# Optimization experiments

Measured on AMD Instinct MI355X. Metric: run time of the kernel, lower is better.

## Reference

```python
import jax, jax.numpy as jnp
import numpy as np


def _diag_perm(h, w):
    # Matches torch loop: offsets -(h-1)..w-1, within offset ordered by row i.
    ii, jj = np.meshgrid(np.arange(h), np.arange(w), indexing='ij')
    idx = np.lexsort((ii.ravel(), (jj - ii).ravel())).astype(np.int32)
    inv = np.argsort(idx).astype(np.int32)
    return jnp.asarray(idx), jnp.asarray(inv)


def _mamba(tok, ln_g, ln_b, Win, conv_w, conv_b, Wx, Wdt, bdt, A_log, Dp, Wout):
    # tok: (B, L, C). MambaLayer = LayerNorm + standard Mamba block.
    di, dc = conv_w.shape
    ds = A_log.shape[-1]
    dtr = Wdt.shape[-1]
    mu = tok.mean(-1, keepdims=True)
    var = ((tok - mu) ** 2).mean(-1, keepdims=True)
    t = (tok - mu) * jax.lax.rsqrt(var + 1e-5) * ln_g + ln_b
    xz = jnp.einsum('blc,ec->ble', t, Win)          # (B,L,2*di)
    xh, z = jnp.split(xz, 2, axis=-1)
    # causal depthwise conv over sequence
    xc = jnp.transpose(xh, (0, 2, 1))               # (B,di,L)
    xc = jax.lax.conv_general_dilated(
        xc, conv_w[:, None, :], (1,), [(dc - 1, 0)],
        dimension_numbers=('NCH', 'OIH', 'NCH'), feature_group_count=di)
    u = jax.nn.silu(jnp.transpose(xc, (0, 2, 1)) + conv_b)  # (B,L,di)
    proj = jnp.einsum('bld,ed->ble', u, Wx)
    dt_r, Bm, Cm = jnp.split(proj, [dtr, dtr + ds], axis=-1)
    dt = jax.nn.softplus(jnp.einsum('blr,dr->bld', dt_r, Wdt) + bdt)  # (B,L,di)
    A = -jnp.exp(A_log)                              # (di,ds)

    def step(h, inp):
        dt_t, B_t, C_t, u_t = inp                    # (B,di) (B,ds) (B,ds) (B,di)
        dA = jnp.exp(dt_t[..., None] * A)            # (B,di,ds)
        h = dA * h + dt_t[..., None] * B_t[:, None, :] * u_t[..., None]
        y = jnp.einsum('bds,bs->bd', h, C_t)
        return h, y

    h0 = jnp.zeros((u.shape[0], di, ds), u.dtype)
    _, ys = jax.lax.scan(step, h0, (jnp.moveaxis(dt, 1, 0), jnp.moveaxis(Bm, 1, 0),
                                    jnp.moveaxis(Cm, 1, 0), jnp.moveaxis(u, 1, 0)))
    y = jnp.moveaxis(ys, 0, 1) + u * Dp              # (B,L,di)
    y = y * jax.nn.silu(z)
    return jnp.einsum('bld,cd->blc', y, Wout)


def _forward(x, ln_g, ln_b, Win, conv_w, conv_b, Wx, Wdt, bdt, A_log, Dp, Wout):
    b, c, h, w = x.shape
    idx, inv = _diag_perm(h, w)

    def mam(d, tok):
        return _mamba(tok, ln_g[d], ln_b[d], Win[d], conv_w[d], conv_b[d],
                      Wx[d], Wdt[d], bdt[d], A_log[d], Dp[d], Wout[d])

    row_tok = x.reshape(b, c, h * w).transpose(0, 2, 1)
    row_feat = mam(0, row_tok).transpose(0, 2, 1).reshape(b, c, h, w)
    col_tok = x.transpose(0, 1, 3, 2).reshape(b, c, w * h).transpose(0, 2, 1)
    col_feat = mam(1, col_tok).transpose(0, 2, 1).reshape(b, c, w, h).transpose(0, 1, 3, 2)
    diag_feat = mam(2, row_tok[:, idx, :])[:, inv, :].transpose(0, 2, 1).reshape(b, c, h, w)
    xf = x[:, :, :, ::-1]
    anti_tok = xf.reshape(b, c, h * w).transpose(0, 2, 1)[:, idx, :]
    anti_feat = mam(3, anti_tok)[:, inv, :].transpose(0, 2, 1).reshape(b, c, h, w)[:, :, :, ::-1]
    gate = jax.nn.sigmoid((row_feat + col_feat + diag_feat + anti_feat) / 4.0)
    return x * gate


def setup_inputs() -> dict:
    key = jax.random.key(0)
    ks = jax.random.split(key, 8)
    B, C, H, W = 4, 96, 48, 48
    DI, DS, DC, DTR = 192, 16, 4, 6
    s = 0.05
    return {
        'x': jax.random.normal(ks[0], (B, C, H, W), jnp.float32),
        'ln_g': jnp.ones((4, C), jnp.float32),
        'ln_b': jnp.zeros((4, C), jnp.float32),
        'Win': jax.random.normal(ks[1], (4, 2 * DI, C), jnp.float32) * s,
        'conv_w': jax.random.normal(ks[2], (4, DI, DC), jnp.float32) * s,
        'conv_b': jnp.zeros((4, DI), jnp.float32),
        'Wx': jax.random.normal(ks[3], (4, DTR + 2 * DS, DI), jnp.float32) * s,
        'Wdt': jax.random.normal(ks[4], (4, DI, DTR), jnp.float32) * s,
        'bdt': jax.random.normal(ks[5], (4, DI), jnp.float32) * s,
        'A_log': jnp.log(jnp.broadcast_to(jnp.arange(1, DS + 1, dtype=jnp.float32), (4, DI, DS))),
        'Dp': jnp.ones((4, DI), jnp.float32),
        'Wout': jax.random.normal(ks[6], (4, C, DI), jnp.float32) * s,
    }


def reference(x, ln_g, ln_b, Win, conv_w, conv_b, Wx, Wdt, bdt, A_log, Dp, Wout):
    return _forward(x, ln_g, ln_b, Win, conv_w, conv_b, Wx, Wdt, bdt, A_log, Dp, Wout)
```

## Files before the change

### kernel.cpp

```cpp
#include <hip/hip_runtime.h>
#include <math.h>

#define LSEQ 2304
#define LC 32
#define NCH 72

typedef unsigned short u16;
typedef unsigned int u32;
typedef __attribute__((ext_vector_type(8))) short bf16x8;
typedef __attribute__((ext_vector_type(4))) float f32x4;

__device__ __forceinline__ float sigmoidf_(float v){ return 1.f/(1.f+__expf(-v)); }
__device__ __forceinline__ u16 f2b(float f){
  union{float f; u32 u;} v; v.f = f;
  u32 r = v.u + 0x7fffu + ((v.u >> 16) & 1u);
  return (u16)(r >> 16);
}
__device__ __forceinline__ float b2f(u16 h){
  union{u32 u; float f;} v; v.u = ((u32)h) << 16; return v.f;
}
__device__ __forceinline__ u16 f2h(float f){
  _Float16 h = (_Float16)f;
  union{_Float16 h; u16 u;} v; v.h = h; return v.u;
}
__device__ __forceinline__ float h2f(u16 u){
  union{u16 u; _Float16 h;} v; v.u = u; return (float)v.h;
}
__device__ __forceinline__ uint2 pack4(float a, float b, float c, float d){
  uint2 o;
  o.x = (u32)f2b(a) | ((u32)f2b(b) << 16);
  o.y = (u32)f2b(c) | ((u32)f2b(d) << 16);
  return o;
}
__device__ __forceinline__ float softplus_(float v){
  return fmaxf(v, 0.f) + __logf(1.f + __expf(-fabsf(v)));
}

__global__ void prep_fold(const float* __restrict__ Win, const float* __restrict__ ln_g,
                          const float* __restrict__ ln_b, const float* __restrict__ A_log,
                          const float* __restrict__ Wout, const float* __restrict__ Wx,
                          const float* __restrict__ Wdt, const float* __restrict__ bdt,
                          u16* __restrict__ WinMF, float* __restrict__ b2,
                          float* __restrict__ Aneg2, u16* __restrict__ WoutMF,
                          u16* __restrict__ Wcomb, float* __restrict__ bcomb,
                          int* __restrict__ g, int* __restrict__ invg, int* __restrict__ flag){
  int i = blockIdx.x * 256 + threadIdx.x;
  if (i < LSEQ){
    int l = i;
    g[l] = l;
    g[LSEQ + l] = (l % 48) * 48 + l / 48;
    invg[l] = l;
    invg[LSEQ + l] = (l % 48) * 48 + l / 48;
    int p = i;
    int ii = p / 48, jj = p % 48, dd = jj - ii;
    int off = (dd <= 0) ? (47 + dd) * (48 + dd) / 2
                        : 1176 + 48 * (dd - 1) - dd * (dd - 1) / 2;
    int l2 = off + min(ii, jj);
    g[2 * LSEQ + l2] = p;
    g[3 * LSEQ + l2] = ii * 48 + 47 - jj;
    invg[2 * LSEQ + p] = l2;
    invg[3 * LSEQ + ii * 48 + 47 - jj] = l2;
  }
  if (i < 4*192*16){
    float a = -expf(A_log[i]);
    Aneg2[i] = a * 1.44269504f;
    int s = i & 15;
    float a0 = -expf(A_log[i - s]);
    if (fabsf(a - (float)(s + 1) * a0) > 1e-5f * fabsf(a) + 1e-30f)
      atomicOr(flag, 1);
  }
  if (i < 4*384*96){
    int d = i / 36864, r = i % 36864, c = r % 96;
    WinMF[i] = f2b(Win[i] * ln_g[d*96 + c]);
  }
  if (i < 4*96*192) WoutMF[i] = f2b(Wout[i]);
  if (i < 4*224*192){
    int d = i / 43008, r = i % 43008, e = r / 192, c = r % 192;
    float w;
    if (e < 192){
      const float* wdt = &Wdt[(size_t)(d*192 + e) * 6];
      w = 0.f;
      #pragma unroll
      for (int r6 = 0; r6 < 6; ++r6) w += wdt[r6] * Wx[(size_t)(d*38 + r6) * 192 + c];
    } else if (e < 208){
      w = Wx[(size_t)(d*38 + 6 + (e - 192)) * 192 + c];
    } else {
      w = Wx[(size_t)(d*38 + 22 + (e - 208)) * 192 + c];
    }
    Wcomb[i] = f2b(w);
  }
  if (i < 4*224){
    int d = i / 224, e = i % 224;
    bcomb[i] = (e < 192) ? bdt[d*192 + e] : 0.f;
  }
  if (i < 4*384){
    int d = i / 384;
    const float* wr = &Win[(size_t)i * 96];
    const float* lb = &ln_b[d * 96];
    float s = 0.f;
    for (int c = 0; c < 96; ++c) s += wr[c] * lb[c];
    b2[i] = s;
  }
}

__global__ __launch_bounds__(256) void ln_kernel(const float* __restrict__ x, u16* __restrict__ n){
  __shared__ float red[512];
  int tid = threadIdx.x;
  int s = tid & 63, q = tid >> 6;
  int T = blockIdx.x * 64 + s;
  int b = T / 2304, p = T % 2304;
  const float* xp = x + (size_t)b * 96 * 2304 + p;
  float vals[24];
  float sum = 0.f, ss = 0.f;
  #pragma unroll
  for (int k = 0; k < 24; ++k){
    float v = xp[(size_t)(q*24 + k) * 2304];
    vals[k] = v; sum += v; ss += v*v;
  }
  red[q*64 + s] = sum;
  red[256 + q*64 + s] = ss;
  __syncthreads();
  float S = red[s] + red[64+s] + red[128+s] + red[192+s];
  float Q = red[256+s] + red[320+s] + red[384+s] + red[448+s];
  float mu = S * (1.f/96.f);
  float var = Q * (1.f/96.f) - mu*mu;
  float rs = rsqrtf(var + 1e-5f);
  u32 w[12];
  #pragma unroll
  for (int k = 0; k < 12; ++k){
    float v0 = (vals[2*k]   - mu) * rs;
    float v1 = (vals[2*k+1] - mu) * rs;
    w[k] = (u32)f2b(v0) | ((u32)f2b(v1) << 16);
  }
  uint4* np_ = (uint4*)(n + (size_t)T * 96 + q*24);
  np_[0] = make_uint4(w[0], w[1], w[2],  w[3]);
  np_[1] = make_uint4(w[4], w[5], w[6],  w[7]);
  np_[2] = make_uint4(w[8], w[9], w[10], w[11]);
}

__global__ __launch_bounds__(256) void kproj(const u16* __restrict__ nbf,
    const u16* __restrict__ WinMF, const float* __restrict__ b2,
    const int* __restrict__ invg, u16* __restrict__ xz, u16* __restrict__ sz){
  int d = blockIdx.y;
  int wv = threadIdx.x >> 6, lane = threadIdx.x & 63;
  int lr = lane & 15, lg = lane >> 4;
  int r0 = blockIdx.x * 64 + wv * 16;
  int row = r0 + lr;
  int b = row / 2304, p = row % 2304;
  const u16* Ap = nbf + (size_t)row * 96 + lg * 8;
  bf16x8 tk0 = *(const bf16x8*)(Ap);
  bf16x8 tk1 = *(const bf16x8*)(Ap + 32);
  bf16x8 tk2 = *(const bf16x8*)(Ap + 64);
  const u16* Wb = WinMF + (size_t)d * 36864 + (size_t)lr * 96 + lg * 8;
  const float* b2d = b2 + d * 384;
  u16* outx = xz + ((size_t)d * 9216 + row) * 192;
  int lseq = invg[d * LSEQ + p];
  u16* outz = sz + ((size_t)(d*4 + b) * LSEQ + lseq) * 192;
  for (int grp = 0; grp < 3; ++grp){
    f32x4 acc[8];
    #pragma unroll
    for (int t = 0; t < 8; ++t)
      acc[t] = *(const f32x4*)&b2d[(grp*8 + t)*16 + lg*4];
    #pragma unroll
    for (int t = 0; t < 8; ++t){
      const u16* wp = Wb + (size_t)(grp*8 + t) * 1536;
      acc[t] = __builtin_amdgcn_mfma_f32_16x16x32_bf16(*(const bf16x8*)(wp     ), tk0, acc[t], 0, 0, 0);
      acc[t] = __builtin_amdgcn_mfma_f32_16x16x32_bf16(*(const bf16x8*)(wp + 32), tk1, acc[t], 0, 0, 0);
      acc[t] = __builtin_amdgcn_mfma_f32_16x16x32_bf16(*(const bf16x8*)(wp + 64), tk2, acc[t], 0, 0, 0);
    }
    #pragma unroll
    for (int t = 0; t < 8; ++t){
      int te = grp*8 + t;
      if (te < 12){
        uint2 o = pack4(acc[t][0], acc[t][1], acc[t][2], acc[t][3]);
        *(uint2*)&outx[te*16 + lg*4] = o;
      } else {
        float z0 = acc[t][0], z1 = acc[t][1], z2 = acc[t][2], z3 = acc[t][3];
        z0 *= sigmoidf_(z0); z1 *= sigmoidf_(z1); z2 *= sigmoidf_(z2); z3 *= sigmoidf_(z3);
        *(uint2*)&outz[(te-12)*16 + lg*4] = pack4(z0, z1, z2, z3);
      }
    }
  }
}

__global__ __launch_bounds__(256) void kconv(const u16* __restrict__ xz, const int* __restrict__ g,
    const float* __restrict__ conv_w, const float* __restrict__ conv_b,
    u16* __restrict__ u){
  __shared__ u16 xh[67][200];
  int d = blockIdx.z, b = blockIdx.y, l0 = blockIdx.x * 64;
  int tid = threadIdx.x;
  const int* gd = g + d * LSEQ;
  const u16* xzd = xz + (size_t)d * 9216 * 192 + (size_t)b * LSEQ * 192;
  for (int i = tid; i < 67*24; i += 256){
    int lt = i / 24, j = i % 24;
    int gl = l0 - 3 + lt;
    uint4 v = make_uint4(0u, 0u, 0u, 0u);
    if (gl >= 0){
      int p = gd[gl];
      v = *(const uint4*)(xzd + (size_t)p * 192 + j * 8);
    }
    *(uint4*)&xh[lt][j*8] = v;
  }
  __syncthreads();
  size_t obase = ((size_t)(d*4 + b) * LSEQ + l0) * 192;
  for (int i = tid; i < 64*48; i += 256){
    int lt = i / 48, j = (i % 48) * 4;
    float a0 = conv_b[d*192 + j + 0];
    float a1 = conv_b[d*192 + j + 1];
    float a2 = conv_b[d*192 + j + 2];
    float a3 = conv_b[d*192 + j + 3];
    const float4 w0 = *(const float4*)&conv_w[(size_t)(d*192 + j + 0) * 4];
    const float4 w1 = *(const float4*)&conv_w[(size_t)(d*192 + j + 1) * 4];
    const float4 w2 = *(const float4*)&conv_w[(size_t)(d*192 + j + 2) * 4];
    const float4 w3 = *(const float4*)&conv_w[(size_t)(d*192 + j + 3) * 4];
    const float* w0p = (const float*)&w0;
    const float* w1p = (const float*)&w1;
    const float* w2p = (const float*)&w2;
    const float* w3p = (const float*)&w3;
    #pragma unroll
    for (int kk = 0; kk < 4; ++kk){
      uint2 xv = *(const uint2*)&xh[lt + kk][j];
      a0 += w0p[kk] * b2f((u16)(xv.x & 0xffff));
      a1 += w1p[kk] * b2f((u16)(xv.x >> 16));
      a2 += w2p[kk] * b2f((u16)(xv.y & 0xffff));
      a3 += w3p[kk] * b2f((u16)(xv.y >> 16));
    }
    a0 *= sigmoidf_(a0); a1 *= sigmoidf_(a1); a2 *= sigmoidf_(a2); a3 *= sigmoidf_(a3);
    *(uint2*)(u + obase + (size_t)lt * 192 + j) = pack4(a0, a1, a2, a3);
  }
}

__global__ __launch_bounds__(256) void kernBM(const u16* __restrict__ u,
    const u16* __restrict__ Wcomb, const float* __restrict__ bcomb,
    u16* __restrict__ dtb, float* __restrict__ Bm, float* __restrict__ Cm){
  __shared__ u16 ush[64 * 200];
  int d = blockIdx.y;
  int tid = threadIdx.x;
  int tile0 = blockIdx.x * 64;
  const u16* ub = u + ((size_t)d * 4 * LSEQ + tile0) * 192;
  for (int i = tid; i < 64*24; i += 256){
    int row = i / 24, c8 = i % 24;
    *(uint4*)&ush[row*200 + c8*8] = *(const uint4*)&ub[(size_t)row*192 + c8*8];
  }
  __syncthreads();
  int wv = tid >> 6, lane = tid & 63;
  int lr = lane & 15, lg = lane >> 4;
  const u16* urow = &ush[(wv*16 + lr)*200 + lg*8];
  bf16x8 tk[6];
  #pragma unroll
  for (int kc = 0; kc < 6; ++kc) tk[kc] = *(const bf16x8*)(urow + kc*32);
  const u16* Wb = Wcomb + (size_t)d * 224 * 192 + (size_t)lr * 192 + lg * 8;
  bf16x8 bw[2][6];
  #pragma unroll
  for (int kc = 0; kc < 6; ++kc) bw[0][kc] = *(const bf16x8*)(Wb + kc*32);
  size_t tokrow = (size_t)d * 4 * LSEQ + tile0 + wv*16 + lr;
  for (int t = 0; t < 14; ++t){
    int cur = t & 1;
    if (t < 13){
      const u16* wp = Wb + (size_t)(t + 1) * 3072;
      #pragma unroll
      for (int kc = 0; kc < 6; ++kc) bw[cur^1][kc] = *(const bf16x8*)(wp + kc*32);
    }
    f32x4 a = (f32x4){0.f, 0.f, 0.f, 0.f};
    #pragma unroll
    for (int kc = 0; kc < 6; ++kc)
      a = __builtin_amdgcn_mfma_f32_16x16x32_bf16(bw[cur][kc], tk[kc], a, 0, 0, 0);
    if (t < 12){
      f32x4 bb = *(const f32x4*)&bcomb[d*224 + t*16 + lg*4];
      float s0 = softplus_(a[0] + bb[0]);
      float s1 = softplus_(a[1] + bb[1]);
      float s2 = softplus_(a[2] + bb[2]);
      float s3 = softplus_(a[3] + bb[3]);
      uint2 o;
      o.x = (u32)f2h(s0) | ((u32)f2h(s1) << 16);
      o.y = (u32)f2h(s2) | ((u32)f2h(s3) << 16);
      *(uint2*)&dtb[tokrow * 192 + t*16 + lg*4] = o;
    } else if (t == 12){
      *(float4*)&Bm[tokrow * 16 + lg*4] = make_float4(a[0], a[1], a[2], a[3]);
    } else {
      *(float4*)&Cm[tokrow * 16 + lg*4] = make_float4(a[0], a[1], a[2], a[3]);
    }
  }
}

__global__ __launch_bounds__(192) void kernC1(const u16* __restrict__ dtb, const u16* __restrict__ u,
    const float* __restrict__ Bm, const float* __restrict__ Cm,
    const float* __restrict__ Aneg2, const int* __restrict__ flag,
    u16* __restrict__ hfin, float* __restrict__ Send, u32* __restrict__ yS){
  __shared__ float Bsh[LC*16];
  __shared__ float Csh[LC*16];
  __shared__ u16 dtsh[LC*192];
  __shared__ u16 ush2[LC*192];
  int ch = blockIdx.x, b = blockIdx.y, d = blockIdx.z;
  int seq = d*4 + b;
  int di = threadIdx.x;
  size_t tb = (size_t)seq * LSEQ + ch * LC;
  const float* bp = Bm + tb * 16;
  const float* cp = Cm + tb * 16;
  for (int i = di; i < LC*16; i += 192){ Bsh[i] = bp[i]; Csh[i] = cp[i]; }
  {
    const uint4* dt4 = (const uint4*)(dtb + tb * 192);
    const uint4* u4  = (const uint4*)(u   + tb * 192);
    #pragma unroll
    for (int i = di; i < LC*24; i += 192){
      *(uint4*)&dtsh[i*8] = dt4[i];
      *(uint4*)&ush2[i*8] = u4[i];
    }
  }
  u32* ySp = yS + tb * 192;
  float h[16];
  #pragma unroll
  for (int s = 0; s < 16; ++s) h[s] = 0.f;
  float Sacc = 0.f;
  __syncthreads();
  if (*flag == 0){
    float A2_0 = Aneg2[(d*192 + di) * 16];
    for (int j = 0; j < LC; ++j){
      float dtv = h2f(dtsh[j*192 + di]);
      float uv  = b2f(ush2[j*192 + di]);
      float Bs[16], Cs[16];
      {
        const float4* b4 = (const float4*)&Bsh[j * 16];
        const float4* c4 = (const float4*)&Csh[j * 16];
        #pragma unroll
        for (int q = 0; q < 4; ++q){
          float4 v = b4[q]; Bs[q*4]=v.x; Bs[q*4+1]=v.y; Bs[q*4+2]=v.z; Bs[q*4+3]=v.w;
          float4 w = c4[q]; Cs[q*4]=w.x; Cs[q*4+1]=w.y; Cs[q*4+2]=w.z; Cs[q*4+3]=w.w;
        }
      }
      float dtu = dtv * uv;
      float e1 = __builtin_amdgcn_exp2f(dtv * A2_0);
      float e2 = e1*e1, e4 = e2*e2, e8 = e4*e4;
      float p[8];
      p[0]=e1; p[1]=e2; p[2]=e1*e2; p[3]=e4; p[4]=e1*e4; p[5]=e2*e4; p[6]=p[2]*e4; p[7]=e8;
      float yv = 0.f;
      #pragma unroll
      for (int s = 0; s < 8; ++s){
        h[s] = p[s]*h[s] + dtu*Bs[s];
        yv += h[s]*Cs[s];
        float q = p[s]*e8;
        h[s+8] = q*h[s+8] + dtu*Bs[s+8];
        yv += h[s+8]*Cs[s+8];
      }
      Sacc += dtv;
      ySp[j*192 + di] = (u32)f2h(yv) | ((u32)f2h(Sacc) << 16);
    }
  } else {
    float A2[16];
    {
      const float4* ap = (const float4*)&Aneg2[(d*192 + di) * 16];
      #pragma unroll
      for (int q = 0; q < 4; ++q){ float4 a4 = ap[q]; A2[q*4]=a4.x; A2[q*4+1]=a4.y; A2[q*4+2]=a4.z; A2[q*4+3]=a4.w; }
    }
    for (int j = 0; j < LC; ++j){
      float dtv = h2f(dtsh[j*192 + di]);
      float uv  = b2f(ush2[j*192 + di]);
      float Bs[16], Cs[16];
      {
        const float4* b4 = (const float4*)&Bsh[j * 16];
        const float4* c4 = (const float4*)&Csh[j * 16];
        #pragma unroll
        for (int q = 0; q < 4; ++q){
          float4 v = b4[q]; Bs[q*4]=v.x; Bs[q*4+1]=v.y; Bs[q*4+2]=v.z; Bs[q*4+3]=v.w;
          float4 w = c4[q]; Cs[q*4]=w.x; Cs[q*4+1]=w.y; Cs[q*4+2]=w.z; Cs[q*4+3]=w.w;
        }
      }
      float dtu = dtv * uv;
      float yv = 0.f;
      #pragma unroll
      for (int s = 0; s < 16; ++s){
        h[s] = __builtin_amdgcn_exp2f(dtv * A2[s]) * h[s] + dtu * Bs[s];
        yv += h[s] * Cs[s];
      }
      Sacc += dtv;
      ySp[j*192 + di] = (u32)f2h(yv) | ((u32)f2h(Sacc) << 16);
    }
  }
  u16* hf = &hfin[((size_t)seq * NCH + ch) * 3072 + di * 16];
  uint4 o0, o1;
  o0.x = (u32)f2b(h[0])  | ((u32)f2b(h[1])  << 16);
  o0.y = (u32)f2b(h[2])  | ((u32)f2b(h[3])  << 16);
  o0.z = (u32)f2b(h[4])  | ((u32)f2b(h[5])  << 16);
  o0.w = (u32)f2b(h[6])  | ((u32)f2b(h[7])  << 16);
  o1.x = (u32)f2b(h[8])  | ((u32)f2b(h[9])  << 16);
  o1.y = (u32)f2b(h[10]) | ((u32)f2b(h[11]) << 16);
  o1.z = (u32)f2b(h[12]) | ((u32)f2b(h[13]) << 16);
  o1.w = (u32)f2b(h[14]) | ((u32)f2b(h[15]) << 16);
  *(uint4*)hf = o0;
  *(uint4*)(hf + 8) = o1;
  Send[((size_t)seq * NCH + ch) * 192 + di] = Sacc;
}

__global__ __launch_bounds__(256) void kernC2(const u16* __restrict__ hfin, const float* __restrict__ Send,
    const float* __restrict__ Aneg2, u16* __restrict__ hin){
  int t = blockIdx.x * 256 + threadIdx.x;
  int seq = t / 3072, q = t % 3072;
  int di = q >> 4, s = q & 15;
  int d = seq >> 2;
  float A2 = Aneg2[(d*192 + di)*16 + s];
  float hr = 0.f;
  const u16* hf = hfin + (size_t)seq * NCH * 3072 + q;
  u16* hi = hin + (size_t)seq * NCH * 3072 + q;
  const float* Se = Send + (size_t)seq * NCH * 192 + di;
  for (int ch = 0; ch < NCH; ch += 8){
    float Se8[8]; u16 hf8[8];
    #pragma unroll
    for (int k = 0; k < 8; ++k){
      Se8[k] = Se[(size_t)(ch+k) * 192];
      hf8[k] = hf[(size_t)(ch+k) * 3072];
    }
    #pragma unroll
    for (int k = 0; k < 8; ++k){
      hi[(size_t)(ch+k) * 3072] = f2b(hr);
      hr = b2f(hf8[k]) + __builtin_amdgcn_exp2f(A2 * Se8[k]) * hr;
    }
  }
}

__global__ __launch_bounds__(384) void kscan2out(const u32* __restrict__ yS, const u16* __restrict__ u,
    const float* __restrict__ Cm,
    const float* __restrict__ Aneg2, const int* __restrict__ flag, const u16* __restrict__ hin,
    const u16* __restrict__ sz, const float* __restrict__ Dp,
    const u16* __restrict__ WoutMF, const int* __restrict__ g,
    u16* __restrict__ feat){
  __shared__ float Csh[64*16];
  __shared__ u16 vsh[64][200];
  int b = blockIdx.y, d = blockIdx.z;
  int seq = d*4 + b;
  int l0 = blockIdx.x * 64;
  int tid = threadIdx.x;
  int gc = tid / 192, di = tid % 192;
  int ch = blockIdx.x * 2 + gc;
  {
    const float* cp = Cm + ((size_t)seq * LSEQ + l0) * 16;
    for (int i = tid; i < 64*16; i += 384) Csh[i] = cp[i];
  }
  float hs[16];
  {
    const uint4* hi4 = (const uint4*)&hin[((size_t)seq * NCH + ch) * 3072 + di * 16];
    uint4 v0 = hi4[0], v1 = hi4[1];
    hs[0]=b2f((u16)(v0.x&0xffff)); hs[1]=b2f((u16)(v0.x>>16));
    hs[2]=b2f((u16)(v0.y&0xffff)); hs[3]=b2f((u16)(v0.y>>16));
    hs[4]=b2f((u16)(v0.z&0xffff)); hs[5]=b2f((u16)(v0.z>>16));
    hs[6]=b2f((u16)(v0.w&0xffff)); hs[7]=b2f((u16)(v0.w>>16));
    hs[8]=b2f((u16)(v1.x&0xffff)); hs[9]=b2f((u16)(v1.x>>16));
    hs[10]=b2f((u16)(v1.y&0xffff)); hs[11]=b2f((u16)(v1.y>>16));
    hs[12]=b2f((u16)(v1.z&0xffff)); hs[13]=b2f((u16)(v1.z>>16));
    hs[14]=b2f((u16)(v1.w&0xffff)); hs[15]=b2f((u16)(v1.w>>16));
  }
  float Dpv = Dp[d*192 + di];
  size_t tb = (size_t)seq * LSEQ + ch * LC;
  const u32* ySp = yS + tb * 192;
  const u16* up  = u   + tb * 192;
  const u16* szp = sz  + tb * 192;
  __syncthreads();
  if (*flag == 0){
    float A2_0 = Aneg2[(d*192 + di) * 16];
    #pragma unroll
    for (int jb = 0; jb < 4; ++jb){
      u32 ys8[8]; u16 uu8[8], zz8[8];
      #pragma unroll
      for (int k = 0; k < 8; ++k){
        int j = jb*8 + k;
        ys8[k] = ySp[j*192 + di];
        uu8[k] = up[j*192 + di];
        zz8[k] = szp[j*192 + di];
      }
      #pragma unroll
      for (int k = 0; k < 8; ++k){
        int j = jb*8 + k;
        float yv = h2f((u16)(ys8[k] & 0xffff));
        float Sc = h2f((u16)(ys8[k] >> 16));
        float uv = b2f(uu8[k]);
        float Cs[16];
        {
          const float4* c4 = (const float4*)&Csh[(gc*32 + j) * 16];
          #pragma unroll
          for (int q = 0; q < 4; ++q){ float4 w = c4[q]; Cs[q*4]=w.x; Cs[q*4+1]=w.y; Cs[q*4+2]=w.z; Cs[q*4+3]=w.w; }
        }
        float e1 = __builtin_amdgcn_exp2f(Sc * A2_0);
        float e2 = e1*e1, e4 = e2*e2, e8 = e4*e4;
        float p[8];
        p[0]=e1; p[1]=e2; p[2]=e1*e2; p[3]=e4; p[4]=e1*e4; p[5]=e2*e4; p[6]=p[2]*e4; p[7]=e8;
        float corr = 0.f;
        #pragma unroll
        for (int s = 0; s < 8; ++s){
          corr += p[s]    * hs[s]   * Cs[s];
          corr += p[s]*e8 * hs[s+8] * Cs[s+8];
        }
        float szv = b2f(zz8[k]);
        vsh[gc*32 + j][di] = f2b((yv + corr + uv * Dpv) * szv);
      }
    }
  } else {
    float A2[16];
    {
      const float4* ap = (const float4*)&Aneg2[(d*192 + di) * 16];
      #pragma unroll
      for (int q = 0; q < 4; ++q){ float4 a4 = ap[q]; A2[q*4]=a4.x; A2[q*4+1]=a4.y; A2[q*4+2]=a4.z; A2[q*4+3]=a4.w; }
    }
    #pragma unroll
    for (int jb = 0; jb < 4; ++jb){
      u32 ys8[8]; u16 uu8[8], zz8[8];
      #pragma unroll
      for (int k = 0; k < 8; ++k){
        int j = jb*8 + k;
        ys8[k] = ySp[j*192 + di];
        uu8[k] = up[j*192 + di];
        zz8[k] = szp[j*192 + di];
      }
      #pragma unroll
      for (int k = 0; k < 8; ++k){
        int j = jb*8 + k;
        float yv = h2f((u16)(ys8[k] & 0xffff));
        float Sc = h2f((u16)(ys8[k] >> 16));
        float uv = b2f(uu8[k]);
        float Cs[16];
        {
          const float4* c4 = (const float4*)&Csh[(gc*32 + j) * 16];
          #pragma unroll
          for (int q = 0; q < 4; ++q){ float4 w = c4[q]; Cs[q*4]=w.x; Cs[q*4+1]=w.y; Cs[q*4+2]=w.z; Cs[q*4+3]=w.w; }
        }
        float corr = 0.f;
        #pragma unroll
        for (int s = 0; s < 16; ++s)
          corr += __builtin_amdgcn_exp2f(Sc * A2[s]) * hs[s] * Cs[s];
        float szv = b2f(zz8[k]);
        vsh[gc*32 + j][di] = f2b((yv + corr + uv * Dpv) * szv);
      }
    }
  }
  __syncthreads();
  if (tid < 256){
    int wv = tid >> 6, lane = tid & 63;
    int lr = lane & 15, lg = lane >> 4;
    bf16x8 tk[6];
    #pragma unroll
    for (int kc = 0; kc < 6; ++kc)
      tk[kc] = *(const bf16x8*)&vsh[wv*16 + lr][kc*32 + lg*8];
    const u16* Wb = WoutMF + (size_t)d * 18432 + (size_t)lr * 192 + lg * 8;
    f32x4 acc[6];
    #pragma unroll
    for (int t = 0; t < 6; ++t) acc[t] = (f32x4){0.f, 0.f, 0.f, 0.f};
    #pragma unroll
    for (int t = 0; t < 6; ++t){
      const u16* wp = Wb + (size_t)t * 3072;
      #pragma unroll
      for (int kc = 0; kc < 6; ++kc)
        acc[t] = __builtin_amdgcn_mfma_f32_16x16x32_bf16(*(const bf16x8*)(wp + kc*32), tk[kc], acc[t], 0, 0, 0);
    }
    u16* fd = feat + (size_t)seq * LSEQ * 96;
    int p = g[d*LSEQ + l0 + wv*16 + lr];
    #pragma unroll
    for (int t = 0; t < 6; ++t){
      uint2 o = pack4(acc[t][0], acc[t][1], acc[t][2], acc[t][3]);
      *(uint2*)&fd[(size_t)p * 96 + t*16 + lg*4] = o;
    }
  }
}

__global__ __launch_bounds__(256) void kernE(const float* __restrict__ x, const u16* __restrict__ feat,
    float* __restrict__ out){
  __shared__ float acc[64 * 97];
  int p0 = blockIdx.x * 64, b = blockIdx.y;
  int tid = threadIdx.x;
  const size_t DS_ = (size_t)4 * LSEQ * 96;
  size_t base = ((size_t)b * LSEQ + p0) * 96;
  for (int i = tid; i < 3072; i += 256){
    int pp = i / 48, c2 = (i % 48) * 2;
    size_t o = base + (size_t)pp * 96 + c2;
    u32 v0 = *(const u32*)(feat + o);
    u32 v1 = *(const u32*)(feat + DS_ + o);
    u32 v2 = *(const u32*)(feat + 2*DS_ + o);
    u32 v3 = *(const u32*)(feat + 3*DS_ + o);
    float s0 = b2f((u16)(v0 & 0xffff)) + b2f((u16)(v1 & 0xffff)) + b2f((u16)(v2 & 0xffff)) + b2f((u16)(v3 & 0xffff));
    float s1 = b2f((u16)(v0 >> 16)) + b2f((u16)(v1 >> 16)) + b2f((u16)(v2 >> 16)) + b2f((u16)(v3 >> 16));
    acc[pp*97 + c2] = s0;
    acc[pp*97 + c2 + 1] = s1;
  }
  __syncthreads();
  for (int i = tid; i < 6144; i += 256){
    int c = i / 64, pp = i % 64;
    size_t o = ((size_t)b * 96 + c) * LSEQ + p0 + pp;
    out[o] = x[o] * sigmoidf_(acc[pp*97 + c] * 0.25f);
  }
}

extern "C" void kernel_launch(void* const* d_in, const int* in_sizes, int n_in,
                              void* d_out, int out_size, void* d_ws, size_t ws_size,
                              hipStream_t stream) {
  const float* x      = (const float*)d_in[0];
  const float* ln_g   = (const float*)d_in[1];
  const float* ln_b   = (const float*)d_in[2];
  const float* Win    = (const float*)d_in[3];
  const float* conv_w = (const float*)d_in[4];
  const float* conv_b = (const float*)d_in[5];
  const float* Wx     = (const float*)d_in[6];
  const float* Wdt    = (const float*)d_in[7];
  const float* bdt    = (const float*)d_in[8];
  const float* A_log  = (const float*)d_in[9];
  const float* Dp     = (const float*)d_in[10];
  const float* Wout   = (const float*)d_in[11];

  char* W = (char*)d_ws;
  char* W0 = W;
  auto alloc = [&](size_t bytes) -> char* {
    char* p = W; W += (bytes + 255) & ~(size_t)255; return p;
  };
  int*   g      = (int*)  alloc((size_t)4 * LSEQ * 4);
  int*   invg   = (int*)  alloc((size_t)4 * LSEQ * 4);
  int*   flag   = (int*)  alloc(256);
  float* Aneg2  = (float*)alloc((size_t)4 * 192 * 16 * 4);
  float* b2     = (float*)alloc((size_t)4 * 384 * 4);
  u16*   WinMF  = (u16*)  alloc((size_t)4 * 384 * 96 * 2);
  u16*   WoutMF = (u16*)  alloc((size_t)4 * 96 * 192 * 2);
  u16*   Wcomb  = (u16*)  alloc((size_t)4 * 224 * 192 * 2);
  float* bcomb  = (float*)alloc((size_t)4 * 224 * 4);
  u16*   nbf    = (u16*)  alloc((size_t)9216 * 96 * 2);
  u16*   xz     = (u16*)  alloc((size_t)4 * 9216 * 192 * 2);
  u16*   ubf    = (u16*)  alloc((size_t)16 * LSEQ * 192 * 2);
  u16*   szbf   = (u16*)  alloc((size_t)16 * LSEQ * 192 * 2);
  u16*   dtb    = (u16*)  alloc((size_t)16 * LSEQ * 192 * 2);
  float* Bm     = (float*)alloc((size_t)16 * LSEQ * 16 * 4);
  float* Cm     = (float*)alloc((size_t)16 * LSEQ * 16 * 4);
  u32*   ySbuf  = (u32*)  alloc((size_t)16 * LSEQ * 192 * 4);
  float* Send   = (float*)alloc((size_t)16 * NCH * 192 * 4);
  u16*   hfin   = (u16*)  alloc((size_t)16 * NCH * 3072 * 2);
  u16*   hin    = (u16*)  alloc((size_t)16 * NCH * 3072 * 2);
  u16*   feat   = (u16*)  alloc((size_t)16 * LSEQ * 96 * 2);
  if ((size_t)(W - W0) > ws_size) return;

  hipMemsetAsync(flag, 0, sizeof(int), stream);
  prep_fold<<<768, 256, 0, stream>>>(Win, ln_g, ln_b, A_log, Wout, Wx, Wdt, bdt,
                                     WinMF, b2, Aneg2, WoutMF, Wcomb, bcomb, g, invg, flag);
  ln_kernel<<<144, 256, 0, stream>>>(x, nbf);
  kproj<<<dim3(144, 4), 256, 0, stream>>>(nbf, WinMF, b2, invg, xz, szbf);
  kconv<<<dim3(36, 4, 4), 256, 0, stream>>>(xz, g, conv_w, conv_b, ubf);
  kernBM<<<dim3(144, 4), 256, 0, stream>>>(ubf, Wcomb, bcomb, dtb, Bm, Cm);
  kernC1<<<dim3(NCH, 4, 4), 192, 0, stream>>>(dtb, ubf, Bm, Cm, Aneg2, flag, hfin, Send, ySbuf);
  kernC2<<<192, 256, 0, stream>>>(hfin, Send, Aneg2, hin);
  kscan2out<<<dim3(36, 4, 4), 384, 0, stream>>>(ySbuf, ubf, Cm, Aneg2, flag, hin, szbf, Dp,
                                                WoutMF, g, feat);
  kernE<<<dim3(36, 4), 256, 0, stream>>>(x, feat, (float*)d_out);
}
```

Before: 181.7 us.

## Fuse layernorm into prep kernel, conv into BM projection, and D-skip into scan

The layernorm kernel is merged into the weight-prep launch as extra blocks. The depthwise conv kernel now feeds its SiLU output straight from shared memory into the dt/B/C MFMA projection, which removes one launch and a global re-read of u. The u*D skip term moves into the chunk scan, so the final scan+output kernel no longer reads u. The cost is a longer fused kernel with more registers and extra block-index branching in prep_fold.

```diff
diff --git a/kernel.cpp b/kernel.cpp
--- a/kernel.cpp
+++ b/kernel.cpp
@@ -36,14 +36,51 @@
   return fmaxf(v, 0.f) + __logf(1.f + __expf(-fabsf(v)));
 }
 
-__global__ void prep_fold(const float* __restrict__ Win, const float* __restrict__ ln_g,
+__global__ __launch_bounds__(256) void prep_fold(const float* __restrict__ Win, const float* __restrict__ ln_g,
                           const float* __restrict__ ln_b, const float* __restrict__ A_log,
                           const float* __restrict__ Wout, const float* __restrict__ Wx,
                           const float* __restrict__ Wdt, const float* __restrict__ bdt,
+                          const float* __restrict__ x,
                           u16* __restrict__ WinMF, float* __restrict__ b2,
                           float* __restrict__ Aneg2, u16* __restrict__ WoutMF,
                           u16* __restrict__ Wcomb, float* __restrict__ bcomb,
-                          int* __restrict__ g, int* __restrict__ invg, int* __restrict__ flag){
+                          int* __restrict__ g, int* __restrict__ invg, int* __restrict__ flag,
+                          u16* __restrict__ n){
+  __shared__ float red[512];
+  if (blockIdx.x >= 768){
+    int tid = threadIdx.x;
+    int s = tid & 63, q = tid >> 6;
+    int T = (blockIdx.x - 768) * 64 + s;
+    int b = T / 2304, p = T % 2304;
+    const float* xp = x + (size_t)b * 96 * 2304 + p;
+    float vals[24];
+    float sum = 0.f, ss = 0.f;
+    #pragma unroll
+    for (int k = 0; k < 24; ++k){
+      float v = xp[(size_t)(q*24 + k) * 2304];
+      vals[k] = v; sum += v; ss += v*v;
+    }
+    red[q*64 + s] = sum;
+    red[256 + q*64 + s] = ss;
+    __syncthreads();
+    float S = red[s] + red[64+s] + red[128+s] + red[192+s];
+    float Q = red[256+s] + red[320+s] + red[384+s] + red[448+s];
+    float mu = S * (1.f/96.f);
+    float var = Q * (1.f/96.f) - mu*mu;
+    float rs = rsqrtf(var + 1e-5f);
+    u32 w[12];
+    #pragma unroll
+    for (int k = 0; k < 12; ++k){
+      float v0 = (vals[2*k]   - mu) * rs;
+      float v1 = (vals[2*k+1] - mu) * rs;
+      w[k] = (u32)f2b(v0) | ((u32)f2b(v1) << 16);
+    }
+    uint4* np_ = (uint4*)(n + (size_t)T * 96 + q*24);
+    np_[0] = make_uint4(w[0], w[1], w[2],  w[3]);
+    np_[1] = make_uint4(w[4], w[5], w[6],  w[7]);
+    np_[2] = make_uint4(w[8], w[9], w[10], w[11]);
+    return;
+  }
   int i = blockIdx.x * 256 + threadIdx.x;
   if (i < LSEQ){
     int l = i;
@@ -101,41 +138,6 @@
     for (int c = 0; c < 96; ++c) s += wr[c] * lb[c];
     b2[i] = s;
   }
-}
-
-__global__ __launch_bounds__(256) void ln_kernel(const float* __restrict__ x, u16* __restrict__ n){
-  __shared__ float red[512];
-  int tid = threadIdx.x;
-  int s = tid & 63, q = tid >> 6;
-  int T = blockIdx.x * 64 + s;
-  int b = T / 2304, p = T % 2304;
-  const float* xp = x + (size_t)b * 96 * 2304 + p;
-  float vals[24];
-  float sum = 0.f, ss = 0.f;
-  #pragma unroll
-  for (int k = 0; k < 24; ++k){
-    float v = xp[(size_t)(q*24 + k) * 2304];
-    vals[k] = v; sum += v; ss += v*v;
-  }
-  red[q*64 + s] = sum;
-  red[256 + q*64 + s] = ss;
-  __syncthreads();
-  float S = red[s] + red[64+s] + red[128+s] + red[192+s];
-  float Q = red[256+s] + red[320+s] + red[384+s] + red[448+s];
-  float mu = S * (1.f/96.f);
-  float var = Q * (1.f/96.f) - mu*mu;
-  float rs = rsqrtf(var + 1e-5f);
-  u32 w[12];
-  #pragma unroll
-  for (int k = 0; k < 12; ++k){
-    float v0 = (vals[2*k]   - mu) * rs;
-    float v1 = (vals[2*k+1] - mu) * rs;
-    w[k] = (u32)f2b(v0) | ((u32)f2b(v1) << 16);
-  }
-  uint4* np_ = (uint4*)(n + (size_t)T * 96 + q*24);
-  np_[0] = make_uint4(w[0], w[1], w[2],  w[3]);
-  np_[1] = make_uint4(w[4], w[5], w[6],  w[7]);
-  np_[2] = make_uint4(w[8], w[9], w[10], w[11]);
 }
 
 __global__ __launch_bounds__(256) void kproj(const u16* __restrict__ nbf,
@@ -183,10 +185,11 @@
   }
 }
 
-__global__ __launch_bounds__(256) void kconv(const u16* __restrict__ xz, const int* __restrict__ g,
+__global__ __launch_bounds__(256) void kconvBM(const u16* __restrict__ xz, const int* __restrict__ g,
     const float* __restrict__ conv_w, const float* __restrict__ conv_b,
-    u16* __restrict__ u){
-  __shared__ u16 xh[67][200];
+    const u16* __restrict__ Wcomb, const float* __restrict__ bcomb,
+    u16* __restrict__ u, u16* __restrict__ dtb, float* __restrict__ Bm, float* __restrict__ Cm){
+  __shared__ u16 xh[67*200];
   int d = blockIdx.z, b = blockIdx.y, l0 = blockIdx.x * 64;
   int tid = threadIdx.x;
   const int* gd = g + d * LSEQ;
@@ -199,11 +202,13 @@
       int p = gd[gl];
       v = *(const uint4*)(xzd + (size_t)p * 192 + j * 8);
     }
-    *(uint4*)&xh[lt][j*8] = v;
+    *(uint4*)&xh[lt*200 + j*8] = v;
   }
   __syncthreads();
-  size_t obase = ((size_t)(d*4 + b) * LSEQ + l0) * 192;
-  for (int i = tid; i < 64*48; i += 256){
+  uint2 ures[12];
+  #pragma unroll
+  for (int it = 0; it < 12; ++it){
+    int i = tid + it*256;
     int lt = i / 48, j = (i % 48) * 4;
     float a0 = conv_b[d*192 + j + 0];
     float a1 = conv_b[d*192 + j + 1];
@@ -219,33 +224,28 @@
     const float* w3p = (const float*)&w3;
     #pragma unroll
     for (int kk = 0; kk < 4; ++kk){
-      uint2 xv = *(const uint2*)&xh[lt + kk][j];
+      uint2 xv = *(const uint2*)&xh[(lt + kk)*200 + j];
       a0 += w0p[kk] * b2f((u16)(xv.x & 0xffff));
       a1 += w1p[kk] * b2f((u16)(xv.x >> 16));
       a2 += w2p[kk] * b2f((u16)(xv.y & 0xffff));
       a3 += w3p[kk] * b2f((u16)(xv.y >> 16));
     }
     a0 *= sigmoidf_(a0); a1 *= sigmoidf_(a1); a2 *= sigmoidf_(a2); a3 *= sigmoidf_(a3);
-    *(uint2*)(u + obase + (size_t)lt * 192 + j) = pack4(a0, a1, a2, a3);
-  }
-}
-
-__global__ __launch_bounds__(256) void kernBM(const u16* __restrict__ u,
-    const u16* __restrict__ Wcomb, const float* __restrict__ bcomb,
-    u16* __restrict__ dtb, float* __restrict__ Bm, float* __restrict__ Cm){
-  __shared__ u16 ush[64 * 200];
-  int d = blockIdx.y;
-  int tid = threadIdx.x;
-  int tile0 = blockIdx.x * 64;
-  const u16* ub = u + ((size_t)d * 4 * LSEQ + tile0) * 192;
-  for (int i = tid; i < 64*24; i += 256){
-    int row = i / 24, c8 = i % 24;
-    *(uint4*)&ush[row*200 + c8*8] = *(const uint4*)&ub[(size_t)row*192 + c8*8];
+    ures[it] = pack4(a0, a1, a2, a3);
+  }
+  __syncthreads();
+  size_t obase = ((size_t)(d*4 + b) * LSEQ + l0) * 192;
+  #pragma unroll
+  for (int it = 0; it < 12; ++it){
+    int i = tid + it*256;
+    int lt = i / 48, j = (i % 48) * 4;
+    *(uint2*)&xh[lt*200 + j] = ures[it];
+    *(uint2*)(u + obase + (size_t)lt * 192 + j) = ures[it];
   }
   __syncthreads();
   int wv = tid >> 6, lane = tid & 63;
   int lr = lane & 15, lg = lane >> 4;
-  const u16* urow = &ush[(wv*16 + lr)*200 + lg*8];
+  const u16* urow = &xh[(wv*16 + lr)*200 + lg*8];
   bf16x8 tk[6];
   #pragma unroll
   for (int kc = 0; kc < 6; ++kc) tk[kc] = *(const bf16x8*)(urow + kc*32);
@@ -253,7 +253,7 @@
   bf16x8 bw[2][6];
   #pragma unroll
   for (int kc = 0; kc < 6; ++kc) bw[0][kc] = *(const bf16x8*)(Wb + kc*32);
-  size_t tokrow = (size_t)d * 4 * LSEQ + tile0 + wv*16 + lr;
+  size_t tokrow = (size_t)(d*4 + b) * LSEQ + l0 + wv*16 + lr;
   for (int t = 0; t < 14; ++t){
     int cur = t & 1;
     if (t < 13){
@@ -285,7 +285,7 @@
 
 __global__ __launch_bounds__(192) void kernC1(const u16* __restrict__ dtb, const u16* __restrict__ u,
     const float* __restrict__ Bm, const float* __restrict__ Cm,
-    const float* __restrict__ Aneg2, const int* __restrict__ flag,
+    const float* __restrict__ Aneg2, const float* __restrict__ Dp, const int* __restrict__ flag,
     u16* __restrict__ hfin, float* __restrict__ Send, u32* __restrict__ yS){
   __shared__ float Bsh[LC*16];
   __shared__ float Csh[LC*16];
@@ -308,6 +308,7 @@
     }
   }
   u32* ySp = yS + tb * 192;
+  float Dpv = Dp[d*192 + di];
   float h[16];
   #pragma unroll
   for (int s = 0; s < 16; ++s) h[s] = 0.f;
@@ -333,7 +334,7 @@
       float e2 = e1*e1, e4 = e2*e2, e8 = e4*e4;
       float p[8];
       p[0]=e1; p[1]=e2; p[2]=e1*e2; p[3]=e4; p[4]=e1*e4; p[5]=e2*e4; p[6]=p[2]*e4; p[7]=e8;
-      float yv = 0.f;
+      float yv = uv * Dpv;
       #pragma unroll
       for (int s = 0; s < 8; ++s){
         h[s] = p[s]*h[s] + dtu*Bs[s];
@@ -366,7 +367,7 @@
         }
       }
       float dtu = dtv * uv;
-      float yv = 0.f;
+      float yv = uv * Dpv;
       #pragma unroll
       for (int s = 0; s < 16; ++s){
         h[s] = __builtin_amdgcn_exp2f(dtv * A2[s]) * h[s] + dtu * Bs[s];
@@ -417,10 +418,10 @@
   }
 }
 
-__global__ __launch_bounds__(384) void kscan2out(const u32* __restrict__ yS, const u16* __restrict__ u,
+__global__ __launch_bounds__(384) void kscan2out(const u32* __restrict__ yS,
     const float* __restrict__ Cm,
     const float* __restrict__ Aneg2, const int* __restrict__ flag, const u16* __restrict__ hin,
-    const u16* __restrict__ sz, const float* __restrict__ Dp,
+    const u16* __restrict__ sz,
     const u16* __restrict__ WoutMF, const int* __restrict__ g,
     u16* __restrict__ feat){
   __shared__ float Csh[64*16];
@@ -448,22 +449,19 @@
     hs[12]=b2f((u16)(v1.z&0xffff)); hs[13]=b2f((u16)(v1.z>>16));
     hs[14]=b2f((u16)(v1.w&0xffff)); hs[15]=b2f((u16)(v1.w>>16));
   }
-  float Dpv = Dp[d*192 + di];
   size_t tb = (size_t)seq * LSEQ + ch * LC;
   const u32* ySp = yS + tb * 192;
-  const u16* up  = u   + tb * 192;
   const u16* szp = sz  + tb * 192;
   __syncthreads();
   if (*flag == 0){
     float A2_0 = Aneg2[(d*192 + di) * 16];
     #pragma unroll
     for (int jb = 0; jb < 4; ++jb){
-      u32 ys8[8]; u16 uu8[8], zz8[8];
+      u32 ys8[8]; u16 zz8[8];
       #pragma unroll
       for (int k = 0; k < 8; ++k){
         int j = jb*8 + k;
         ys8[k] = ySp[j*192 + di];
-        uu8[k] = up[j*192 + di];
         zz8[k] = szp[j*192 + di];
       }
       #pragma unroll
@@ -471,7 +469,6 @@
         int j = jb*8 + k;
         float yv = h2f((u16)(ys8[k] & 0xffff));
         float Sc = h2f((u16)(ys8[k] >> 16));
-        float uv = b2f(uu8[k]);
         float Cs[16];
         {
           const float4* c4 = (const float4*)&Csh[(gc*32 + j) * 16];
@@ -489,7 +486,7 @@
           corr += p[s]*e8 * hs[s+8] * Cs[s+8];
         }
         float szv = b2f(zz8[k]);
-        vsh[gc*32 + j][di] = f2b((yv + corr + uv * Dpv) * szv);
+        vsh[gc*32 + j][di] = f2b((yv + corr) * szv);
       }
     }
   } else {
@@ -501,12 +498,11 @@
     }
     #pragma unroll
     for (int jb = 0; jb < 4; ++jb){
-      u32 ys8[8]; u16 uu8[8], zz8[8];
+      u32 ys8[8]; u16 zz8[8];
       #pragma unroll
       for (int k = 0; k < 8; ++k){
         int j = jb*8 + k;
         ys8[k] = ySp[j*192 + di];
-        uu8[k] = up[j*192 + di];
         zz8[k] = szp[j*192 + di];
       }
       #pragma unroll
@@ -514,7 +510,6 @@
         int j = jb*8 + k;
         float yv = h2f((u16)(ys8[k] & 0xffff));
         float Sc = h2f((u16)(ys8[k] >> 16));
-        float uv = b2f(uu8[k]);
         float Cs[16];
         {
           const float4* c4 = (const float4*)&Csh[(gc*32 + j) * 16];
@@ -526,7 +521,7 @@
         for (int s = 0; s < 16; ++s)
           corr += __builtin_amdgcn_exp2f(Sc * A2[s]) * hs[s] * Cs[s];
         float szv = b2f(zz8[k]);
-        vsh[gc*32 + j][di] = f2b((yv + corr + uv * Dpv) * szv);
+        vsh[gc*32 + j][di] = f2b((yv + corr) * szv);
       }
     }
   }
@@ -631,15 +626,14 @@
   if ((size_t)(W - W0) > ws_size) return;
 
   hipMemsetAsync(flag, 0, sizeof(int), stream);
-  prep_fold<<<768, 256, 0, stream>>>(Win, ln_g, ln_b, A_log, Wout, Wx, Wdt, bdt,
-                                     WinMF, b2, Aneg2, WoutMF, Wcomb, bcomb, g, invg, flag);
-  ln_kernel<<<144, 256, 0, stream>>>(x, nbf);
+  prep_fold<<<912, 256, 0, stream>>>(Win, ln_g, ln_b, A_log, Wout, Wx, Wdt, bdt, x,
+                                     WinMF, b2, Aneg2, WoutMF, Wcomb, bcomb, g, invg, flag, nbf);
   kproj<<<dim3(144, 4), 256, 0, stream>>>(nbf, WinMF, b2, invg, xz, szbf);
-  kconv<<<dim3(36, 4, 4), 256, 0, stream>>>(xz, g, conv_w, conv_b, ubf);
-  kernBM<<<dim3(144, 4), 256, 0, stream>>>(ubf, Wcomb, bcomb, dtb, Bm, Cm);
-  kernC1<<<dim3(NCH, 4, 4), 192, 0, stream>>>(dtb, ubf, Bm, Cm, Aneg2, flag, hfin, Send, ySbuf);
+  kconvBM<<<dim3(36, 4, 4), 256, 0, stream>>>(xz, g, conv_w, conv_b, Wcomb, bcomb,
+                                              ubf, dtb, Bm, Cm);
+  kernC1<<<dim3(NCH, 4, 4), 192, 0, stream>>>(dtb, ubf, Bm, Cm, Aneg2, Dp, flag, hfin, Send, ySbuf);
   kernC2<<<192, 256, 0, stream>>>(hfin, Send, Aneg2, hin);
-  kscan2out<<<dim3(36, 4, 4), 384, 0, stream>>>(ySbuf, ubf, Cm, Aneg2, flag, hin, szbf, Dp,
+  kscan2out<<<dim3(36, 4, 4), 384, 0, stream>>>(ySbuf, Cm, Aneg2, flag, hin, szbf,
                                                 WoutMF, g, feat);
   kernE<<<dim3(36, 4), 256, 0, stream>>>(x, feat, (float*)d_out);
 }
```

Measured after the change: 173.9 us. -4.2%, faster.
